# Optimization experiments

Measured on AMD Instinct MI355X. Metric: run time of the kernel, lower is better.

## Reference

```python
import jax, jax.numpy as jnp
import numpy as np
from jax import lax

KERNEL_SIZES = (3, 5, 7)
EPS = 1e-12  # torch F.normalize default eps


def _gamma(x, k):
    """SpatialCorrelationSampler(kernel_size=k)(x, F.normalize(x, dim=1)).

    With patch_size=1, stride=1, padding=0, dilation=1 the sampler output at
    (b, y, x) is sum over channels and the kxk window of in1 * in2. Since
    in2 = in1 / max(||in1||_c, eps), the channel contraction collapses to
    ||x||^2 / max(||x||, eps) per pixel, followed by a kxk box-sum (VALID).
    x: [B, C, H, W] -> gamma: [B, H-k+1, W-k+1]
    """
    norm = jnp.sqrt(jnp.sum(x * x, axis=1))          # [B, H, W]
    p = (norm * norm) / jnp.maximum(norm, EPS)       # [B, H, W]
    return lax.reduce_window(p, 0.0, lax.add, (1, k, k), (1, 1, 1), 'VALID')


def reference(out_feat0, out_feat1, gt_feat0, gt_feat1):
    loss = jnp.float32(0.0)
    for xo, xg in ((out_feat0, gt_feat0), (out_feat1, gt_feat1)):
        for k in KERNEL_SIZES:
            go = _gamma(xo, k)
            gg = _gamma(xg, k)
            loss = loss + jnp.mean((go - gg) ** 2)   # nn.MSELoss (mean)
    return loss


def setup_inputs() -> dict:
    key = jax.random.key(0)
    k0, k1, k2, k3 = jax.random.split(key, 4)
    return {
        'out_feat0': jax.random.normal(k0, (8, 256, 64, 64), dtype=jnp.float32),
        'out_feat1': jax.random.normal(k1, (8, 512, 32, 32), dtype=jnp.float32),
        'gt_feat0': jax.random.normal(k2, (8, 256, 64, 64), dtype=jnp.float32),
        'gt_feat1': jax.random.normal(k3, (8, 512, 32, 32), dtype=jnp.float32),
    }
```

## Files before the change

kernel.cpp:

```cpp
#include <hip/hip_runtime.h>
#include <math.h>

#define EPS 1e-12f

typedef float f4 __attribute__((ext_vector_type(4)));

template <int W, int C, int H>
__device__ __forceinline__ void row_kernel(
    const float* __restrict__ xo, const float* __restrict__ xg,
    float* __restrict__ r,
    int bh, int tid,
    float* lds  ,
    float* part ,
    float* drow )
{
    constexpr int NT     = 512;
    constexpr int QUADS  = W / 4;
    constexpr int CCHUNK = NT / QUADS;
    constexpr int CPT    = C / CCHUNK;
    constexpr int NR     = 8 * H;
    static_assert(CPT % 4 == 0, "batch-4 load loop");
    static_assert(CCHUNK % 4 == 0, "4-way sub-reduce");

    const int quad = tid % QUADS;
    const int cgrp = tid / QUADS;
    const int b    = bh / H;
    const int h    = bh % H;

    const int plane = H * W;
    const int base  = b * C * plane + h * W + quad * 4;
    const int c0    = cgrp * CPT;

    f4 so = {0.f, 0.f, 0.f, 0.f};
    f4 sg = {0.f, 0.f, 0.f, 0.f};
#pragma unroll
    for (int ib = 0; ib < CPT / 4; ++ib) {
        f4 vo[4], vg[4];
#pragma unroll
        for (int u = 0; u < 4; ++u) {
            const int off = base + (c0 + ib * 4 + u) * plane;
            vo[u] = __builtin_nontemporal_load(reinterpret_cast<const f4*>(xo + off));
            vg[u] = __builtin_nontemporal_load(reinterpret_cast<const f4*>(xg + off));
        }
#pragma unroll
        for (int u = 0; u < 4; ++u) {
            so += vo[u] * vo[u];
            sg += vg[u] * vg[u];
        }
    }

    *reinterpret_cast<f4*>(lds + (0 * CCHUNK + cgrp) * W + quad * 4) = so;
    *reinterpret_cast<f4*>(lds + (1 * CCHUNK + cgrp) * W + quad * 4) = sg;
    __syncthreads();

    constexpr int GPS = CCHUNK / 4;
    if (tid < 8 * W) {
        const int w    = tid % W;
        const int slot = (tid / W) & 1;
        const int sub  = tid / (2 * W);
        float a = 0.f;
#pragma unroll
        for (int g = 0; g < GPS; ++g)
            a += lds[(slot * CCHUNK + sub * GPS + g) * W + w];
        part[(sub * 2 + slot) * W + w] = a;
    }
    __syncthreads();

    if (tid < W) {
        float ao = 0.f, ag = 0.f;
#pragma unroll
        for (int s = 0; s < 4; ++s) {
            ao += part[(s * 2 + 0) * W + tid];
            ag += part[(s * 2 + 1) * W + tid];
        }
        const float no = sqrtf(ao);
        const float ng = sqrtf(ag);
        const float po = ao / fmaxf(no, EPS);
        const float pg = ag / fmaxf(ng, EPS);
        drow[tid] = po - pg;
    }
    __syncthreads();

#pragma unroll
    for (int ki = 0; ki < 3; ++ki) {
        const int k = 3 + 2 * ki;
        const int V = W - k + 1;
        if (tid < V) {
            float s = 0.f;
#pragma unroll
            for (int j = 0; j < 7; ++j)
                if (j < k) s += drow[tid + j];
            r[(ki * NR + bh) * W + tid] = s;
        }
    }
}

__global__ __launch_bounds__(512) void stage1_kernel(
    const float* __restrict__ o0, const float* __restrict__ g0,
    const float* __restrict__ o1, const float* __restrict__ g1,
    float* __restrict__ r0, float* __restrict__ r1,
    float* __restrict__ out)
{
    __shared__ float lds[4096];
    __shared__ float part[512];
    __shared__ float drow[64];
    const int bid = blockIdx.x;
    if (bid == 0 && threadIdx.x == 0) out[0] = 0.0f;
    if (bid < 8 * 64) {
        row_kernel<64, 256, 64>(o0, g0, r0, bid, threadIdx.x, lds, part, drow);
    } else {
        row_kernel<32, 512, 32>(o1, g1, r1, bid - 8 * 64, threadIdx.x, lds, part, drow);
    }
}

__global__ __launch_bounds__(256) void boxmse_kernel(
    const float* __restrict__ r0, const float* __restrict__ r1,
    float* __restrict__ out)
{
    __shared__ float img[64 * 62];
    __shared__ float wsum[4];

    const int bid = blockIdx.x;
    const int t   = bid / 24;
    const int rem = bid % 24;
    const int b   = rem / 3;
    const int ki  = rem % 3;
    const int k   = 3 + 2 * ki;
    const int H   = (t == 0) ? 64 : 32;
    const int V   = H - k + 1;
    const float* src = ((t == 0) ? r0 : r1) + (ki * (8 * H) + b * H) * H;

    const int tid = threadIdx.x;

    for (int i = tid; i < H * V; i += 256) {
        const int y = i / V;
        const int x = i - y * V;
        img[i] = src[y * H + x];
    }
    __syncthreads();

    float acc = 0.f;
    for (int i = tid; i < V * V; i += 256) {
        const int y = i / V;
        const int x = i - y * V;
        float s = 0.f;
        for (int j = 0; j < k; ++j) s += img[(y + j) * V + x];
        acc = fmaf(s, s, acc);
    }

    for (int off = 32; off > 0; off >>= 1) acc += __shfl_down(acc, off);
    if ((tid & 63) == 0) wsum[tid >> 6] = acc;
    __syncthreads();
    if (tid == 0) {
        const float total = wsum[0] + wsum[1] + wsum[2] + wsum[3];
        const float inv_count = 1.0f / (float)(8 * V * V);
        atomicAdd(out, total * inv_count);
    }
}

extern "C" void kernel_launch(void* const* d_in, const int* in_sizes, int n_in,
                              void* d_out, int out_size, void* d_ws, size_t ws_size,
                              hipStream_t stream) {
    const float* out_feat0 = (const float*)d_in[0];
    const float* out_feat1 = (const float*)d_in[1];
    const float* gt_feat0  = (const float*)d_in[2];
    const float* gt_feat1  = (const float*)d_in[3];
    float* out = (float*)d_out;

    float* r0 = (float*)d_ws;
    float* r1 = r0 + 3 * 512 * 64;

    stage1_kernel<<<8 * 64 + 8 * 32, 512, 0, stream>>>(
        out_feat0, gt_feat0, out_feat1, gt_feat1, r0, r1, out);
    boxmse_kernel<<<48, 256, 0, stream>>>(r0, r1, out);
}
```

Measured before the change: 128.7 us.

## Split channel reduction across blocks and move norm/row box-sum into stage 2

Stage 1 now has each block reduce a 256-pixel contiguous slab over a channel slice, writing partial sums of squares to workspace. The norm, difference and row box-sum move into stage 2, which first sums the channel-slice partials per pixel. The point is to make stage-1 global loads contiguous 1KB rows per channel and to shrink the in-block reduction and sync tail. In exchange stage 2 does more work with only 48 blocks and reads a larger partial buffer.

```diff
diff --git a/kernel.cpp b/kernel.cpp
--- a/kernel.cpp
+++ b/kernel.cpp
@@ -5,31 +5,21 @@
 
 typedef float f4 __attribute__((ext_vector_type(4)));
 
-template <int W, int C, int H>
-__device__ __forceinline__ void row_kernel(
+template <int PLANE, int C, int CS_N>
+__device__ __forceinline__ void partial_tile(
     const float* __restrict__ xo, const float* __restrict__ xg,
-    float* __restrict__ r,
-    int bh, int tid,
-    float* lds  ,
-    float* part ,
-    float* drow )
+    float* __restrict__ part,
+    int b, int tile, int cs, int tid, float* lds )
 {
-    constexpr int NT     = 512;
-    constexpr int QUADS  = W / 4;
-    constexpr int CCHUNK = NT / QUADS;
-    constexpr int CPT    = C / CCHUNK;
-    constexpr int NR     = 8 * H;
-    static_assert(CPT % 4 == 0, "batch-4 load loop");
-    static_assert(CCHUNK % 4 == 0, "4-way sub-reduce");
+    constexpr int SLABF = 256;
+    constexpr int CG    = 8;
+    constexpr int CPT   = (C / CS_N) / CG;
+    static_assert(CPT == 8, "geometry");
 
-    const int quad = tid % QUADS;
-    const int cgrp = tid / QUADS;
-    const int b    = bh / H;
-    const int h    = bh % H;
-
-    const int plane = H * W;
-    const int base  = b * C * plane + h * W + quad * 4;
-    const int c0    = cgrp * CPT;
+    const int quad = tid & 63;
+    const int cg   = tid >> 6;
+    const int base = b * C * PLANE + tile * SLABF + quad * 4;
+    const int c0   = cs * (C / CS_N) + cg * CPT;
 
     f4 so = {0.f, 0.f, 0.f, 0.f};
     f4 sg = {0.f, 0.f, 0.f, 0.f};
@@ -38,7 +28,7 @@
         f4 vo[4], vg[4];
 #pragma unroll
         for (int u = 0; u < 4; ++u) {
-            const int off = base + (c0 + ib * 4 + u) * plane;
+            const int off = base + (c0 + ib * 4 + u) * PLANE;
             vo[u] = __builtin_nontemporal_load(reinterpret_cast<const f4*>(xo + off));
             vg[u] = __builtin_nontemporal_load(reinterpret_cast<const f4*>(xg + off));
         }
@@ -49,75 +39,47 @@
         }
     }
 
-    *reinterpret_cast<f4*>(lds + (0 * CCHUNK + cgrp) * W + quad * 4) = so;
-    *reinterpret_cast<f4*>(lds + (1 * CCHUNK + cgrp) * W + quad * 4) = sg;
+    *reinterpret_cast<f4*>(lds + (0 * CG + cg) * SLABF + quad * 4) = so;
+    *reinterpret_cast<f4*>(lds + (1 * CG + cg) * SLABF + quad * 4) = sg;
     __syncthreads();
 
-    constexpr int GPS = CCHUNK / 4;
-    if (tid < 8 * W) {
-        const int w    = tid % W;
-        const int slot = (tid / W) & 1;
-        const int sub  = tid / (2 * W);
-        float a = 0.f;
+    if (tid < 128) {
+        const int s = tid >> 6;
+        const int q = tid & 63;
+        f4 a = {0.f, 0.f, 0.f, 0.f};
 #pragma unroll
-        for (int g = 0; g < GPS; ++g)
-            a += lds[(slot * CCHUNK + sub * GPS + g) * W + w];
-        part[(sub * 2 + slot) * W + w] = a;
-    }
-    __syncthreads();
-
-    if (tid < W) {
-        float ao = 0.f, ag = 0.f;
-#pragma unroll
-        for (int s = 0; s < 4; ++s) {
-            ao += part[(s * 2 + 0) * W + tid];
-            ag += part[(s * 2 + 1) * W + tid];
-        }
-        const float no = sqrtf(ao);
-        const float ng = sqrtf(ag);
-        const float po = ao / fmaxf(no, EPS);
-        const float pg = ag / fmaxf(ng, EPS);
-        drow[tid] = po - pg;
-    }
-    __syncthreads();
-
-#pragma unroll
-    for (int ki = 0; ki < 3; ++ki) {
-        const int k = 3 + 2 * ki;
-        const int V = W - k + 1;
-        if (tid < V) {
-            float s = 0.f;
-#pragma unroll
-            for (int j = 0; j < 7; ++j)
-                if (j < k) s += drow[tid + j];
-            r[(ki * NR + bh) * W + tid] = s;
-        }
+        for (int g = 0; g < CG; ++g)
+            a += *reinterpret_cast<const f4*>(lds + (s * CG + g) * SLABF + q * 4);
+        *reinterpret_cast<f4*>(
+            part + ((s * 8 + b) * CS_N + cs) * PLANE + tile * SLABF + q * 4) = a;
     }
 }
 
-__global__ __launch_bounds__(512) void stage1_kernel(
+__global__ __launch_bounds__(512) void stage1a_kernel(
     const float* __restrict__ o0, const float* __restrict__ g0,
     const float* __restrict__ o1, const float* __restrict__ g1,
-    float* __restrict__ r0, float* __restrict__ r1,
+    float* __restrict__ part0, float* __restrict__ part1,
     float* __restrict__ out)
 {
     __shared__ float lds[4096];
-    __shared__ float part[512];
-    __shared__ float drow[64];
     const int bid = blockIdx.x;
     if (bid == 0 && threadIdx.x == 0) out[0] = 0.0f;
-    if (bid < 8 * 64) {
-        row_kernel<64, 256, 64>(o0, g0, r0, bid, threadIdx.x, lds, part, drow);
+    if (bid < 512) {
+        const int b = bid >> 6, tile = (bid >> 2) & 15, cs = bid & 3;
+        partial_tile<4096, 256, 4>(o0, g0, part0, b, tile, cs, threadIdx.x, lds);
     } else {
-        row_kernel<32, 512, 32>(o1, g1, r1, bid - 8 * 64, threadIdx.x, lds, part, drow);
+        const int e = bid - 512;
+        const int b = e >> 5, tile = (e >> 3) & 3, cs = e & 7;
+        partial_tile<1024, 512, 8>(o1, g1, part1, b, tile, cs, threadIdx.x, lds);
     }
 }
 
-__global__ __launch_bounds__(256) void boxmse_kernel(
-    const float* __restrict__ r0, const float* __restrict__ r1,
+__global__ __launch_bounds__(256) void stage2_kernel(
+    const float* __restrict__ part0, const float* __restrict__ part1,
     float* __restrict__ out)
 {
-    __shared__ float img[64 * 62];
+    __shared__ float d[4096];
+    __shared__ float rbuf[64 * 62];
     __shared__ float wsum[4];
 
     const int bid = blockIdx.x;
@@ -126,16 +88,40 @@
     const int b   = rem / 3;
     const int ki  = rem % 3;
     const int k   = 3 + 2 * ki;
-    const int H   = (t == 0) ? 64 : 32;
+    const int H   = t ? 32 : 64;
     const int V   = H - k + 1;
-    const float* src = ((t == 0) ? r0 : r1) + (ki * (8 * H) + b * H) * H;
+    const int PLANE = H * H;
+    const int CS  = t ? 8 : 4;
+    const float* pb = t ? part1 : part0;
+    const int tid = threadIdx.x;
 
-    const int tid = threadIdx.x;
+    const float* po = pb + (0 * 8 + b) * CS * PLANE;
+    const float* pg = pb + (1 * 8 + b) * CS * PLANE;
+
+    for (int q = tid; q < PLANE / 4; q += 256) {
+        f4 ao = {0.f, 0.f, 0.f, 0.f};
+        f4 ag = {0.f, 0.f, 0.f, 0.f};
+        for (int c = 0; c < CS; ++c) {
+            ao += *reinterpret_cast<const f4*>(po + c * PLANE + q * 4);
+            ag += *reinterpret_cast<const f4*>(pg + c * PLANE + q * 4);
+        }
+        f4 dd;
+#pragma unroll
+        for (int j = 0; j < 4; ++j) {
+            const float no = sqrtf(ao[j]);
+            const float ng = sqrtf(ag[j]);
+            dd[j] = ao[j] / fmaxf(no, EPS) - ag[j] / fmaxf(ng, EPS);
+        }
+        *reinterpret_cast<f4*>(d + q * 4) = dd;
+    }
+    __syncthreads();
 
     for (int i = tid; i < H * V; i += 256) {
         const int y = i / V;
         const int x = i - y * V;
-        img[i] = src[y * H + x];
+        float s = 0.f;
+        for (int j = 0; j < k; ++j) s += d[y * H + x + j];
+        rbuf[i] = s;
     }
     __syncthreads();
 
@@ -144,7 +130,7 @@
         const int y = i / V;
         const int x = i - y * V;
         float s = 0.f;
-        for (int j = 0; j < k; ++j) s += img[(y + j) * V + x];
+        for (int j = 0; j < k; ++j) s += rbuf[(y + j) * V + x];
         acc = fmaf(s, s, acc);
     }
 
@@ -153,8 +139,7 @@
     __syncthreads();
     if (tid == 0) {
         const float total = wsum[0] + wsum[1] + wsum[2] + wsum[3];
-        const float inv_count = 1.0f / (float)(8 * V * V);
-        atomicAdd(out, total * inv_count);
+        atomicAdd(out, total / (float)(8 * V * V));
     }
 }
 
@@ -167,10 +152,10 @@
     const float* gt_feat1  = (const float*)d_in[3];
     float* out = (float*)d_out;
 
-    float* r0 = (float*)d_ws;
-    float* r1 = r0 + 3 * 512 * 64;
+    float* part0 = (float*)d_ws;
+    float* part1 = part0 + 2 * 8 * 4 * 4096;
 
-    stage1_kernel<<<8 * 64 + 8 * 32, 512, 0, stream>>>(
-        out_feat0, gt_feat0, out_feat1, gt_feat1, r0, r1, out);
-    boxmse_kernel<<<48, 256, 0, stream>>>(r0, r1, out);
+    stage1a_kernel<<<768, 512, 0, stream>>>(
+        out_feat0, gt_feat0, out_feat1, gt_feat1, part0, part1, out);
+    stage2_kernel<<<48, 256, 0, stream>>>(part0, part1, out);
 }
```

Measured after the change: 138.3 us. 1.07x slower.
